# Kernel tuning notes

Hardware: AMD Instinct MI355X
Metric: run time of the kernel (lower is better)

## Reference

```python
import jax, jax.numpy as jnp
import numpy as np

EPS_BN = 1e-5
EPS_LN = 1e-5

def _bn(x, gamma, beta, ch_axis):
    # training-mode BatchNorm: batch stats over all axes except ch_axis (biased var)
    axes = tuple(i for i in range(x.ndim) if i != ch_axis)
    mean = x.mean(axes, keepdims=True)
    var = x.var(axes, keepdims=True)
    shp = [1] * x.ndim; shp[ch_axis] = -1
    return (x - mean) / jnp.sqrt(var + EPS_BN) * gamma.reshape(shp) + beta.reshape(shp)

def _ln(x, gamma, beta):
    mean = x.mean(-1, keepdims=True)
    var = x.var(-1, keepdims=True)
    return (x - mean) / jnp.sqrt(var + EPS_LN) * gamma + beta

def _spline(x, knots, cps):
    # x: (B,S); knots, cps: (K,). Single-pass bucketize + gather + lerp,
    # equivalent to the torch per-interval masked loop (boundary points take
    # the right interval's t=0 value, identical result).
    K = knots.shape[0]
    xn = (x - jnp.min(x)) / (jnp.max(x) - jnp.min(x) + 1e-6)
    idx = jnp.clip(jnp.searchsorted(knots, xn, side='right') - 1, 0, K - 2)
    k0, k1 = knots[idx], knots[idx + 1]
    t = (xn - k0) / (k1 - k0)
    val = (1.0 - t) * cps[idx] + t * cps[idx + 1]
    in_range = (xn >= knots[0]) & (xn <= knots[-1])
    return jnp.where(in_range, val, 0.0)

def _mha(x, in_w, in_b, out_w, out_b, H):
    # torch nn.MultiheadAttention with batch_first=False: dim0 is the sequence.
    L, N, D = x.shape
    hd = D // H
    qkv = x @ in_w.T + in_b                       # (L,N,3D)
    q, k, v = jnp.split(qkv, 3, axis=-1)
    q = q.reshape(L, N, H, hd) * (1.0 / np.sqrt(hd))
    k = k.reshape(L, N, H, hd)
    v = v.reshape(L, N, H, hd)
    scores = jnp.einsum('lnhd,mnhd->nhlm', q, k)  # (N,H,L,L)
    attn = jax.nn.softmax(scores, axis=-1)
    out = jnp.einsum('nhlm,mnhd->lnhd', attn, v).reshape(L, N, D)
    return out @ out_w.T + out_b

def setup_inputs() -> dict:
    B, S, D, F, K, H = 32, 1024, 512, 8, 32, 8
    key = jax.random.key(0)
    ks = jax.random.split(key, 12)
    s = 0.02
    inp = {
        'x': jax.random.normal(ks[0], (B, S, D), jnp.float32),
        'in_w': jax.random.normal(ks[1], (3 * D, D), jnp.float32) * s,
        'in_b': jnp.zeros((3 * D,), jnp.float32),
        'out_w': jax.random.normal(ks[2], (D, D), jnp.float32) * s,
        'out_b': jnp.zeros((D,), jnp.float32),
        'attn_g': jnp.ones((D,), jnp.float32),
        'attn_beta': jnp.zeros((D,), jnp.float32),
        'proj_w': jax.random.normal(ks[3], (F, D), jnp.float32) * s,
        'proj_b': jnp.zeros((F,), jnp.float32),
        'pn_g': jnp.ones((F,), jnp.float32),
        'pn_beta': jnp.zeros((F,), jnp.float32),
        'knots': jnp.tile(jnp.linspace(0.0, 1.0, K, dtype=jnp.float32)[None, :], (F, 1)),
        'cps': jax.random.normal(ks[4], (F, K), jnp.float32) / np.sqrt(K),
        'gate_w': jax.random.normal(ks[5], (2 * D, F), jnp.float32) * s,
        'gate_b': jnp.zeros((2 * D,), jnp.float32),
        'gbn_g': jnp.ones((S,), jnp.float32),   # BatchNorm1d(2*d_model) hits dim1 = seq (= 2*d_model)
        'gbn_beta': jnp.zeros((S,), jnp.float32),
        'ln_g': jnp.ones((D,), jnp.float32),
        'ln_beta': jnp.zeros((D,), jnp.float32),
        'outp_w': jax.random.normal(ks[6], (D, D), jnp.float32) * s,
        'outp_b': jnp.zeros((D,), jnp.float32),
        'on_g': jnp.ones((D,), jnp.float32),
        'on_beta': jnp.zeros((D,), jnp.float32),
    }
    return inp

def reference(x, in_w, in_b, out_w, out_b, attn_g, attn_beta, proj_w, proj_b,
              pn_g, pn_beta, knots, cps, gate_w, gate_b, gbn_g, gbn_beta,
              ln_g, ln_beta, outp_w, outp_b, on_g, on_beta):
    H = 8
    attn_out = _mha(x, in_w, in_b, out_w, out_b, H)          # (B,S,D)
    attn_out = _bn(attn_out, attn_g, attn_beta, 2)
    projected = x @ proj_w.T + proj_b                         # (B,S,F)
    projected = _bn(projected, pn_g, pn_beta, 2)
    transformed = jax.vmap(_spline, in_axes=(2, 0, 0), out_axes=2)(projected, knots, cps)  # (B,S,F)
    h = transformed @ gate_w.T + gate_b                       # (B,S,2D)
    h = _bn(h, gbn_g, gbn_beta, 1)                            # channel axis = seq (torch quirk)
    a, b = jnp.split(h, 2, axis=-1)
    glu = a * jax.nn.sigmoid(b)                               # (B,S,D)
    gated = _ln(glu, ln_g, ln_beta)
    out = gated @ outp_w.T + outp_b
    out = _bn(out, on_g, on_beta, 2)
    return x + attn_out + out
```

## Files before the change

### kernel.cpp

```cpp
#include <hip/hip_runtime.h>
#include <math.h>


#define SOFF_AMEAN 0
#define SOFF_ARSTD 512
#define SOFF_OMEAN 1024
#define SOFF_ORSTD 1536
#define SOFF_PMEAN 2048
#define SOFF_PRSTD 2056
#define SOFF_FMIN  2064
#define SOFF_FMAX  2072
#define SOFF_SMEAN 2080
#define SOFF_SRSTD 3104
#define SOFF_G1    4128
#define SOFF_GB    4136
#define SOFF_SGB   4144
#define SOFF_QGB   4145
#define SOFF_G2    4160
#define SOFF_PART  4224

typedef short bf16x8_t __attribute__((ext_vector_type(8)));
typedef float f32x4_t __attribute__((ext_vector_type(4)));
typedef unsigned short us8_t __attribute__((ext_vector_type(8)));

__device__ __forceinline__ unsigned short f2bf(float f) {
  unsigned u = __float_as_uint(f);
  u = (u + 0x7FFFu + ((u >> 16) & 1u)) >> 16;
  return (unsigned short)u;
}
__device__ __forceinline__ float b2f(unsigned short u) {
  return __uint_as_float(((unsigned)u) << 16);
}

__global__ __launch_bounds__(256) void zero_kernel(float* __restrict__ p) {
  p[blockIdx.x * 256 + threadIdx.x] = 0.f;
}

__global__ __launch_bounds__(256) void cvt8_kernel(const float* __restrict__ src,
                                                   unsigned short* __restrict__ dst) {
  int i = blockIdx.x * 256 + threadIdx.x;
  float4 a = ((const float4*)src)[i * 2];
  float4 b = ((const float4*)src)[i * 2 + 1];
  us8_t o;
  o[0] = f2bf(a.x); o[1] = f2bf(a.y); o[2] = f2bf(a.z); o[3] = f2bf(a.w);
  o[4] = f2bf(b.x); o[5] = f2bf(b.y); o[6] = f2bf(b.z); o[7] = f2bf(b.w);
  *(us8_t*)(dst + (size_t)i * 8) = o;
}

template<int NT, bool OUT_BF16, bool STATS>
__global__ __launch_bounds__(256) void gemm_mfma_kernel(
    const unsigned short* __restrict__ A, const unsigned short* __restrict__ B,
    const float* __restrict__ bias, unsigned short* __restrict__ Cb,
    float* __restrict__ Cf, float* __restrict__ gstats, int N) {
  __shared__ unsigned short As[128 * 32];
  __shared__ unsigned short Bs[128 * 32];
  __shared__ float colred[256];
  const int bi = blockIdx.x;
  const int xcd = bi & 7, j = bi >> 3;
  const int m0 = (xcd * 32 + j / NT) * 128;
  const int n0 = (j % NT) * 128;
  const int t = threadIdx.x;
  const int w = t >> 6, lane = t & 63;
  const int wm = w >> 1, wn = w & 1;
  if (STATS) colred[t] = 0.f;
  f32x4_t acc[4][4];
#pragma unroll
  for (int i = 0; i < 4; ++i)
#pragma unroll
    for (int jj = 0; jj < 4; ++jj) acc[i][jj] = (f32x4_t){0.f, 0.f, 0.f, 0.f};

  const int lrow = lane >> 2;
  const int lk = (lane & 3) * 8;
  const unsigned short* ga = A + (size_t)(m0 + w * 32 + lrow) * 512 + lk;
  const unsigned short* gb = B + (size_t)(n0 + w * 32 + lrow) * 512 + lk;
  unsigned short* lA = &As[(w * 32) * 32];
  unsigned short* lB = &Bs[(w * 32) * 32];
  const int fr = lane & 15, fq = (lane >> 4) * 8;

  for (int k0 = 0; k0 < 512; k0 += 32) {
    __syncthreads();
    __builtin_amdgcn_global_load_lds(
        (const __attribute__((address_space(1))) void*)(ga + k0),
        (__attribute__((address_space(3))) void*)lA, 16, 0, 0);
    __builtin_amdgcn_global_load_lds(
        (const __attribute__((address_space(1))) void*)(ga + k0 + 16 * 512),
        (__attribute__((address_space(3))) void*)(lA + 16 * 32), 16, 0, 0);
    __builtin_amdgcn_global_load_lds(
        (const __attribute__((address_space(1))) void*)(gb + k0),
        (__attribute__((address_space(3))) void*)lB, 16, 0, 0);
    __builtin_amdgcn_global_load_lds(
        (const __attribute__((address_space(1))) void*)(gb + k0 + 16 * 512),
        (__attribute__((address_space(3))) void*)(lB + 16 * 32), 16, 0, 0);
    __syncthreads();
    bf16x8_t af[4], bf[4];
#pragma unroll
    for (int mi = 0; mi < 4; ++mi)
      af[mi] = *(const bf16x8_t*)&As[(wm * 64 + mi * 16 + fr) * 32 + fq];
#pragma unroll
    for (int ni = 0; ni < 4; ++ni)
      bf[ni] = *(const bf16x8_t*)&Bs[(wn * 64 + ni * 16 + fr) * 32 + fq];
#pragma unroll
    for (int mi = 0; mi < 4; ++mi)
#pragma unroll
      for (int ni = 0; ni < 4; ++ni)
        acc[mi][ni] = __builtin_amdgcn_mfma_f32_16x16x32_bf16(af[mi], bf[ni], acc[mi][ni], 0, 0, 0);
  }
  const int cr = (lane >> 4) * 4, cc = lane & 15;
#pragma unroll
  for (int ni = 0; ni < 4; ++ni) {
    int col = n0 + wn * 64 + ni * 16 + cc;
    float bv = bias[col];
    float lsum = 0.f, lsq = 0.f;
#pragma unroll
    for (int mi = 0; mi < 4; ++mi) {
#pragma unroll
      for (int jj = 0; jj < 4; ++jj) {
        int row = m0 + wm * 64 + mi * 16 + cr + jj;
        float v = acc[mi][ni][jj] + bv;
        if (OUT_BF16) Cb[(size_t)row * N + col] = f2bf(v);
        else          Cf[(size_t)row * N + col] = v;
        if (STATS) { lsum += v; lsq += v * v; }
      }
    }
    if (STATS) {
      lsum += __shfl_xor(lsum, 16); lsum += __shfl_xor(lsum, 32);
      lsq  += __shfl_xor(lsq, 16);  lsq  += __shfl_xor(lsq, 32);
      if (lane < 16) {
        int cidx = wn * 64 + ni * 16 + lane;
        atomicAdd(&colred[cidx], lsum);
        atomicAdd(&colred[128 + cidx], lsq);
      }
    }
  }
  if (STATS) {
    __syncthreads();
    if (t < 128) {
      atomicAdd(&gstats[n0 + t], colred[t]);
      atomicAdd(&gstats[512 + n0 + t], colred[128 + t]);
    }
  }
}

__global__ __launch_bounds__(512) void statsfin_kernel(const float* __restrict__ part,
                                                       float* __restrict__ stats, int off) {
  int t = threadIdx.x;
  float mean = part[t] / 32768.f;
  float var = part[512 + t] / 32768.f - mean * mean;
  stats[off + t] = mean;
  stats[off + 512 + t] = rsqrtf(var + 1e-5f);
}

__global__ __launch_bounds__(256) void attn2_kernel(const unsigned short* __restrict__ qkv,
                                                    unsigned short* __restrict__ ctxb) {
  const int n = blockIdx.x, h = blockIdx.y, t = threadIdx.x;
  __shared__ float qs[32 * 68], ks[32 * 68], vs[32 * 68], ss[32 * 33];
  const int l = t >> 3, j0 = (t & 7) * 8;
  size_t rowb = ((size_t)(l * 1024 + n)) * 1536 + h * 64 + j0;
  us8_t qv = *(const us8_t*)(qkv + rowb);
  us8_t kv = *(const us8_t*)(qkv + rowb + 512);
  us8_t vv = *(const us8_t*)(qkv + rowb + 1024);
#pragma unroll
  for (int j = 0; j < 8; ++j) {
    qs[l * 68 + j0 + j] = b2f(qv[j]) * 0.125f;
    ks[l * 68 + j0 + j] = b2f(kv[j]);
    vs[l * 68 + j0 + j] = b2f(vv[j]);
  }
  __syncthreads();
  for (int o = t; o < 1024; o += 256) {
    int ll = o >> 5, m = o & 31;
    const float4* q4 = (const float4*)&qs[ll * 68];
    const float4* k4 = (const float4*)&ks[m * 68];
    float s = 0.f;
#pragma unroll
    for (int dd = 0; dd < 16; ++dd) {
      float4 a = q4[dd], b = k4[dd];
      s += a.x * b.x + a.y * b.y + a.z * b.z + a.w * b.w;
    }
    ss[ll * 33 + m] = s;
  }
  __syncthreads();
  if (t < 32) {
    float mx = -3e38f;
    for (int m = 0; m < 32; ++m) mx = fmaxf(mx, ss[t * 33 + m]);
    float sum = 0.f;
    for (int m = 0; m < 32; ++m) { float e = __expf(ss[t * 33 + m] - mx); ss[t * 33 + m] = e; sum += e; }
    float inv = 1.f / sum;
    for (int m = 0; m < 32; ++m) ss[t * 33 + m] *= inv;
  }
  __syncthreads();
  float o[8] = {0.f, 0.f, 0.f, 0.f, 0.f, 0.f, 0.f, 0.f};
#pragma unroll 8
  for (int m = 0; m < 32; ++m) {
    float pm = ss[l * 33 + m];
    const float* vr = &vs[m * 68 + j0];
#pragma unroll
    for (int j = 0; j < 8; ++j) o[j] += pm * vr[j];
  }
  us8_t ov;
#pragma unroll
  for (int j = 0; j < 8; ++j) ov[j] = f2bf(o[j]);
  *(us8_t*)(ctxb + ((size_t)(l * 1024 + n)) * 512 + h * 64 + j0) = ov;
}

__global__ __launch_bounds__(256) void proj_kernel(const float* __restrict__ x,
    const float* __restrict__ pw, const float* __restrict__ pb, float* __restrict__ p) {
  int blk = blockIdx.x, t = threadIdx.x;
  int r0 = blk * 64;
  __shared__ float xsp[64 * 33];
  __shared__ float pwc[8 * 33];
  int l = t >> 2, fg = t & 3;
  float acc0 = 0.f, acc1 = 0.f;
  for (int k0 = 0; k0 < 512; k0 += 32) {
    __syncthreads();
    for (int i = t; i < 2048; i += 256) { int ll = i >> 5, kk = i & 31; xsp[ll * 33 + kk] = x[(size_t)(r0 + ll) * 512 + k0 + kk]; }
    { int ff = t >> 5, kk = t & 31; pwc[ff * 33 + kk] = pw[ff * 512 + k0 + kk]; }
    __syncthreads();
#pragma unroll 8
    for (int kk = 0; kk < 32; ++kk) {
      float xv = xsp[l * 33 + kk];
      acc0 += xv * pwc[(fg * 2) * 33 + kk];
      acc1 += xv * pwc[(fg * 2 + 1) * 33 + kk];
    }
  }
  float2 o; o.x = acc0 + pb[fg * 2]; o.y = acc1 + pb[fg * 2 + 1];
  *(float2*)&p[(r0 + l) * 8 + fg * 2] = o;
}

__global__ __launch_bounds__(256) void projstats_kernel(const float* __restrict__ p,
                                                        float* __restrict__ part) {
  int t = threadIdx.x, blk = blockIdx.x;
  int f = t & 7;
  float s = 0.f, s2 = 0.f;
  for (int r = blk * 32 + (t >> 3); r < 32768; r += 2048) { float v = p[r * 8 + f]; s += v; s2 += v * v; }
  __shared__ float red[256], red2[256];
  red[t] = s; red2[t] = s2; __syncthreads();
  for (int off = 128; off >= 8; off >>= 1) { if (t < off) { red[t] += red[t + off]; red2[t] += red2[t + off]; } __syncthreads(); }
  if (t < 8) { part[blk * 16 + t] = red[t]; part[blk * 16 + 8 + t] = red2[t]; }
}
__global__ void projfin_kernel(const float* __restrict__ part, float* __restrict__ stats) {
  int t = threadIdx.x;
  if (t < 8) {
    float s = 0.f, s2 = 0.f;
    for (int b = 0; b < 64; ++b) { s += part[b * 16 + t]; s2 += part[b * 16 + 8 + t]; }
    float mean = s / 32768.f;
    float var = s2 / 32768.f - mean * mean;
    stats[SOFF_PMEAN + t] = mean;
    stats[SOFF_PRSTD + t] = rsqrtf(var + 1e-5f);
  }
}

__global__ __launch_bounds__(256) void bnminmax_kernel(float* __restrict__ p,
    const float* __restrict__ stats, const float* __restrict__ png,
    const float* __restrict__ pnb, float* __restrict__ part) {
  int t = threadIdx.x, blk = blockIdx.x;
  int i0 = blk * 256 + t;
  int f = i0 & 7;
  float k1 = stats[SOFF_PRSTD + f] * png[f];
  float k0 = pnb[f] - stats[SOFF_PMEAN + f] * k1;
  float mn = 3e38f, mx = -3e38f;
  for (int i = i0; i < 262144; i += 16384) {
    float v = p[i] * k1 + k0;
    p[i] = v;
    mn = fminf(mn, v); mx = fmaxf(mx, v);
  }
  __shared__ float rmn[256], rmx[256];
  rmn[t] = mn; rmx[t] = mx; __syncthreads();
  for (int off = 128; off >= 8; off >>= 1) {
    if (t < off) { rmn[t] = fminf(rmn[t], rmn[t + off]); rmx[t] = fmaxf(rmx[t], rmx[t + off]); }
    __syncthreads();
  }
  if (t < 8) { part[blk * 16 + t] = rmn[t]; part[blk * 16 + 8 + t] = rmx[t]; }
}
__global__ void minmaxfin_kernel(const float* __restrict__ part, float* __restrict__ stats) {
  int t = threadIdx.x;
  if (t < 8) {
    float mn = 3e38f, mx = -3e38f;
    for (int b = 0; b < 64; ++b) { mn = fminf(mn, part[b * 16 + t]); mx = fmaxf(mx, part[b * 16 + 8 + t]); }
    stats[SOFF_FMIN + t] = mn;
    stats[SOFF_FMAX + t] = mx;
  }
}

__global__ __launch_bounds__(256) void spline_kernel(float* __restrict__ p,
    const float* __restrict__ knots, const float* __restrict__ cps,
    const float* __restrict__ stats) {
  __shared__ float ksh[8 * 33], csh[8 * 33];
  int t = threadIdx.x;
  { int f = t >> 5, j = t & 31; ksh[f * 33 + j] = knots[t]; csh[f * 33 + j] = cps[t]; }
  __syncthreads();
  int i = blockIdx.x * 256 + t;
  int f = i & 7;
  float xv = p[i];
  float mn = stats[SOFF_FMIN + f], mx = stats[SOFF_FMAX + f];
  float xn = (xv - mn) / (mx - mn + 1e-6f);
  const float* kn = &ksh[f * 33];
  const float* cp = &csh[f * 33];
  int pcnt = 0;
#pragma unroll
  for (int j = 0; j < 32; ++j) pcnt += (kn[j] <= xn) ? 1 : 0;
  int idx = pcnt - 1;
  idx = idx < 0 ? 0 : (idx > 30 ? 30 : idx);
  float k0v = kn[idx], k1v = kn[idx + 1];
  float tt = (xn - k0v) / (k1v - k0v);
  float val = (1.f - tt) * cp[idx] + tt * cp[idx + 1];
  bool inr = (xn >= kn[0]) && (xn <= kn[31]);
  p[i] = inr ? val : 0.f;
}

__global__ __launch_bounds__(256) void gateprep_kernel(const float* __restrict__ gw,
    const float* __restrict__ gb, float* __restrict__ stats) {
  int b = blockIdx.x, t = threadIdx.x;
  __shared__ float red[256];
  float s = 0.f;
  if (b < 64) {
    int f1 = b >> 3, f2 = b & 7;
    for (int j = t; j < 1024; j += 256) s += gw[j * 8 + f1] * gw[j * 8 + f2];
  } else if (b < 72) {
    int f = b - 64;
    for (int j = t; j < 1024; j += 256) s += gw[j * 8 + f];
  } else if (b < 80) {
    int f = b - 72;
    for (int j = t; j < 1024; j += 256) s += gb[j] * gw[j * 8 + f];
  } else if (b == 80) {
    for (int j = t; j < 1024; j += 256) s += gb[j];
  } else {
    for (int j = t; j < 1024; j += 256) s += gb[j] * gb[j];
  }
  red[t] = s; __syncthreads();
  for (int off = 128; off > 0; off >>= 1) { if (t < off) red[t] += red[t + off]; __syncthreads(); }
  if (t == 0) {
    float v = red[0];
    if (b < 64) stats[SOFF_G2 + b] = v;
    else if (b < 72) stats[SOFF_G1 + (b - 64)] = v;
    else if (b < 80) stats[SOFF_GB + (b - 72)] = v;
    else if (b == 80) stats[SOFF_SGB] = v;
    else stats[SOFF_QGB] = v;
  }
}

__global__ __launch_bounds__(256) void sstats_kernel(const float* __restrict__ tbuf,
                                                     float* __restrict__ stats) {
  int s = blockIdx.x, t = threadIdx.x;
  __shared__ float tv[256];
  __shared__ float red[256];
  __shared__ float T1[8];
  __shared__ float Ms[64];
  int b = t >> 3, f = t & 7;
  tv[t] = tbuf[(b * 1024 + s) * 8 + f];
  __syncthreads();
  red[t] = tv[t]; __syncthreads();
  for (int off = 128; off >= 8; off >>= 1) { if (t < off) red[t] += red[t + off]; __syncthreads(); }
  if (t < 8) T1[t] = red[t];
  if (t < 64) {
    int f1 = t >> 3, f2 = t & 7; float sM = 0.f;
    for (int bb = 0; bb < 32; ++bb) sM += tv[bb * 8 + f1] * tv[bb * 8 + f2];
    Ms[t] = sM;
  }
  __syncthreads();
  if (t == 0) {
    float sh = 0.f, s2 = 0.f;
    for (int ff = 0; ff < 8; ++ff) {
      sh += stats[SOFF_G1 + ff] * T1[ff];
      s2 += 2.f * stats[SOFF_GB + ff] * T1[ff];
    }
    sh += 32.f * stats[SOFF_SGB];
    for (int i = 0; i < 64; ++i) s2 += Ms[i] * stats[SOFF_G2 + i];
    s2 += 32.f * stats[SOFF_QGB];
    float mean = sh / 32768.f;
    float var = s2 / 32768.f - mean * mean;
    stats[SOFF_SMEAN + s] = mean;
    stats[SOFF_SRSTD + s] = rsqrtf(var + 1e-5f);
  }
}

__global__ __launch_bounds__(256) void gluln_kernel(const float* __restrict__ tbuf,
    const float* __restrict__ gw, const float* __restrict__ gb,
    const float* __restrict__ stats, const float* __restrict__ gbng,
    const float* __restrict__ gbnb, const float* __restrict__ lng,
    const float* __restrict__ lnb, unsigned short* __restrict__ gatedb) {
  const int t = threadIdx.x, wave = t >> 6, lane = t & 63;
  for (int rr = 0; rr < 4; ++rr) {
    const int r = blockIdx.x * 16 + wave * 4 + rr;
    const int s = r & 1023;
    float4 tA = *(const float4*)&tbuf[r * 8];
    float4 tB = *(const float4*)&tbuf[r * 8 + 4];
    float smean = stats[SOFF_SMEAN + s], srstd = stats[SOFF_SRSTD + s];
    float k1 = srstd * gbng[s];
    float k0 = gbnb[s] - smean * k1;
    float g[8];
    float sum = 0.f, sq = 0.f;
#pragma unroll
    for (int i = 0; i < 8; ++i) {
      int c = i * 64 + lane;
      float4 wa0 = *(const float4*)&gw[c * 8];
      float4 wa1 = *(const float4*)&gw[c * 8 + 4];
      float4 wb0 = *(const float4*)&gw[(c + 512) * 8];
      float4 wb1 = *(const float4*)&gw[(c + 512) * 8 + 4];
      float ha = tA.x * wa0.x + tA.y * wa0.y + tA.z * wa0.z + tA.w * wa0.w
               + tB.x * wa1.x + tB.y * wa1.y + tB.z * wa1.z + tB.w * wa1.w + gb[c];
      float hb = tA.x * wb0.x + tA.y * wb0.y + tA.z * wb0.z + tA.w * wb0.w
               + tB.x * wb1.x + tB.y * wb1.y + tB.z * wb1.z + tB.w * wb1.w + gb[c + 512];
      ha = ha * k1 + k0;
      hb = hb * k1 + k0;
      float gv = ha / (1.f + __expf(-hb));
      g[i] = gv; sum += gv; sq += gv * gv;
    }
#pragma unroll
    for (int m = 32; m >= 1; m >>= 1) { sum += __shfl_xor(sum, m); sq += __shfl_xor(sq, m); }
    float mean = sum * (1.f / 512.f);
    float rstd = rsqrtf(sq * (1.f / 512.f) - mean * mean + 1e-5f);
#pragma unroll
    for (int i = 0; i < 8; ++i) {
      int c = i * 64 + lane;
      gatedb[(size_t)r * 512 + c] = f2bf((g[i] - mean) * rstd * lng[c] + lnb[c]);
    }
  }
}

__global__ __launch_bounds__(256) void final_kernel(const float* __restrict__ x,
    const float* __restrict__ attn, const float* __restrict__ outl,
    const float* __restrict__ stats, const float* __restrict__ ag,
    const float* __restrict__ ab, const float* __restrict__ og,
    const float* __restrict__ ob, float* __restrict__ y) {
  int idx = blockIdx.x * 256 + threadIdx.x;
  int c4 = (idx & 127) * 4;
  float4 xv = ((const float4*)x)[idx];
  float4 av = ((const float4*)attn)[idx];
  float4 ov = ((const float4*)outl)[idx];
  float4 am = *(const float4*)&stats[SOFF_AMEAN + c4];
  float4 ar = *(const float4*)&stats[SOFF_ARSTD + c4];
  float4 om = *(const float4*)&stats[SOFF_OMEAN + c4];
  float4 orr = *(const float4*)&stats[SOFF_ORSTD + c4];
  float4 g1 = *(const float4*)&ag[c4];
  float4 b1 = *(const float4*)&ab[c4];
  float4 g2 = *(const float4*)&og[c4];
  float4 b2 = *(const float4*)&ob[c4];
  float4 o;
  o.x = xv.x + (av.x - am.x) * ar.x * g1.x + b1.x + (ov.x - om.x) * orr.x * g2.x + b2.x;
  o.y = xv.y + (av.y - am.y) * ar.y * g1.y + b1.y + (ov.y - om.y) * orr.y * g2.y + b2.y;
  o.z = xv.z + (av.z - am.z) * ar.z * g1.z + b1.z + (ov.z - om.z) * orr.z * g2.z + b2.z;
  o.w = xv.w + (av.w - am.w) * ar.w * g1.w + b1.w + (ov.w - om.w) * orr.w * g2.w + b2.w;
  ((float4*)y)[idx] = o;
}

extern "C" void kernel_launch(void* const* d_in, const int* in_sizes, int n_in,
                              void* d_out, int out_size, void* d_ws, size_t ws_size,
                              hipStream_t stream) {
  (void)in_sizes; (void)n_in; (void)out_size; (void)ws_size;
  const float* x        = (const float*)d_in[0];
  const float* in_w     = (const float*)d_in[1];
  const float* in_b     = (const float*)d_in[2];
  const float* out_w    = (const float*)d_in[3];
  const float* out_b    = (const float*)d_in[4];
  const float* attn_g   = (const float*)d_in[5];
  const float* attn_bt  = (const float*)d_in[6];
  const float* proj_w   = (const float*)d_in[7];
  const float* proj_b   = (const float*)d_in[8];
  const float* pn_g     = (const float*)d_in[9];
  const float* pn_bt    = (const float*)d_in[10];
  const float* knots    = (const float*)d_in[11];
  const float* cps      = (const float*)d_in[12];
  const float* gate_w   = (const float*)d_in[13];
  const float* gate_b   = (const float*)d_in[14];
  const float* gbn_g    = (const float*)d_in[15];
  const float* gbn_bt   = (const float*)d_in[16];
  const float* ln_g     = (const float*)d_in[17];
  const float* ln_bt    = (const float*)d_in[18];
  const float* outp_w   = (const float*)d_in[19];
  const float* outp_b   = (const float*)d_in[20];
  const float* on_g     = (const float*)d_in[21];
  const float* on_bt    = (const float*)d_in[22];

  float* out = (float*)d_out;
  unsigned short* xb      = (unsigned short*)d_ws;
  unsigned short* qkv_b   = xb + 16777216;
  unsigned short* ctx_b   = qkv_b + 50331648;
  unsigned short* wqkv_b  = ctx_b + 16777216;
  unsigned short* wout_b  = wqkv_b + 786432;
  unsigned short* woutp_b = wout_b + 262144;
  float* proj  = (float*)(woutp_b + 262144);
  float* stats = proj + 262144;
  float* part  = stats + SOFF_PART;
  float* partA  = part;
  float* partO  = part + 1024;
  float* partP  = part + 2048;
  float* partMM = part + 3072;
  float* attnf = (float*)qkv_b;
  unsigned short* gated_b = xb;

  zero_kernel<<<dim3(8), dim3(256), 0, stream>>>(part);
  cvt8_kernel<<<dim3(8192), dim3(256), 0, stream>>>(x, xb);
  cvt8_kernel<<<dim3(384), dim3(256), 0, stream>>>(in_w, wqkv_b);
  cvt8_kernel<<<dim3(128), dim3(256), 0, stream>>>(out_w, wout_b);
  cvt8_kernel<<<dim3(128), dim3(256), 0, stream>>>(outp_w, woutp_b);
  gemm_mfma_kernel<12, true, false><<<dim3(3072), dim3(256), 0, stream>>>(
      xb, wqkv_b, in_b, qkv_b, nullptr, nullptr, 1536);
  attn2_kernel<<<dim3(1024, 8), dim3(256), 0, stream>>>(qkv_b, ctx_b);
  gemm_mfma_kernel<4, false, true><<<dim3(1024), dim3(256), 0, stream>>>(
      ctx_b, wout_b, out_b, nullptr, attnf, partA, 512);
  statsfin_kernel<<<dim3(1), dim3(512), 0, stream>>>(partA, stats, SOFF_AMEAN);
  proj_kernel<<<dim3(512), dim3(256), 0, stream>>>(x, proj_w, proj_b, proj);
  projstats_kernel<<<dim3(64), dim3(256), 0, stream>>>(proj, partP);
  projfin_kernel<<<dim3(1), dim3(64), 0, stream>>>(partP, stats);
  bnminmax_kernel<<<dim3(64), dim3(256), 0, stream>>>(proj, stats, pn_g, pn_bt, partMM);
  minmaxfin_kernel<<<dim3(1), dim3(64), 0, stream>>>(partMM, stats);
  spline_kernel<<<dim3(1024), dim3(256), 0, stream>>>(proj, knots, cps, stats);
  gateprep_kernel<<<dim3(88), dim3(256), 0, stream>>>(gate_w, gate_b, stats);
  sstats_kernel<<<dim3(1024), dim3(256), 0, stream>>>(proj, stats);
  gluln_kernel<<<dim3(2048), dim3(256), 0, stream>>>(proj, gate_w, gate_b, stats,
                                                     gbn_g, gbn_bt, ln_g, ln_bt, gated_b);
  gemm_mfma_kernel<4, false, true><<<dim3(1024), dim3(256), 0, stream>>>(
      gated_b, woutp_b, outp_b, nullptr, out, partO, 512);
  statsfin_kernel<<<dim3(1), dim3(512), 0, stream>>>(partO, stats, SOFF_OMEAN);
  final_kernel<<<dim3(16384), dim3(256), 0, stream>>>(x, attnf, out, stats,
                                                      attn_g, attn_bt, on_g, on_bt, out);
}
```

Baseline: 520.3 us.

## Merge prep launches, fold stat finalizers into consumers, swizzle GEMM LDS reads

Replaces the zero kernel and four convert kernels with a single prep kernel that uses block ranges. Removes the separate statistics-finalisation launches: projection sums are accumulated with atomics inside proj_kernel, min/max is reduced inside spline_kernel, and BN mean/rstd are computed inline in bnminmax and final_kernel. Adds an XOR swizzle on the k offset for GEMM LDS stores and fragment reads to reduce bank conflicts. The final residual now reads the bf16 copy of x instead of fp32 x, which halves that traffic but adds rounding error to the output.

```diff
diff --git a/kernel.cpp b/kernel.cpp
--- a/kernel.cpp
+++ b/kernel.cpp
@@ -2,14 +2,6 @@
 #include <math.h>
 
 
-#define SOFF_AMEAN 0
-#define SOFF_ARSTD 512
-#define SOFF_OMEAN 1024
-#define SOFF_ORSTD 1536
-#define SOFF_PMEAN 2048
-#define SOFF_PRSTD 2056
-#define SOFF_FMIN  2064
-#define SOFF_FMAX  2072
 #define SOFF_SMEAN 2080
 #define SOFF_SRSTD 3104
 #define SOFF_G1    4128
@@ -32,18 +24,23 @@
   return __uint_as_float(((unsigned)u) << 16);
 }
 
-__global__ __launch_bounds__(256) void zero_kernel(float* __restrict__ p) {
-  p[blockIdx.x * 256 + threadIdx.x] = 0.f;
-}
-
-__global__ __launch_bounds__(256) void cvt8_kernel(const float* __restrict__ src,
-                                                   unsigned short* __restrict__ dst) {
-  int i = blockIdx.x * 256 + threadIdx.x;
+__global__ __launch_bounds__(256) void prep_kernel(const float* __restrict__ x,
+    const float* __restrict__ in_w, const float* __restrict__ out_w,
+    const float* __restrict__ outp_w, unsigned short* __restrict__ xb,
+    unsigned short* __restrict__ wqkv, unsigned short* __restrict__ wout,
+    unsigned short* __restrict__ woutp, float* __restrict__ part) {
+  int b = blockIdx.x, t = threadIdx.x;
+  const float* src; unsigned short* dst; int i;
+  if (b < 8192)      { src = x;      dst = xb;    i = b * 256 + t; }
+  else if (b < 8576) { src = in_w;   dst = wqkv;  i = (b - 8192) * 256 + t; }
+  else if (b < 8704) { src = out_w;  dst = wout;  i = (b - 8576) * 256 + t; }
+  else if (b < 8832) { src = outp_w; dst = woutp; i = (b - 8704) * 256 + t; }
+  else { ((float4*)part)[(b - 8832) * 256 + t] = (float4){0.f, 0.f, 0.f, 0.f}; return; }
   float4 a = ((const float4*)src)[i * 2];
-  float4 b = ((const float4*)src)[i * 2 + 1];
+  float4 c = ((const float4*)src)[i * 2 + 1];
   us8_t o;
   o[0] = f2bf(a.x); o[1] = f2bf(a.y); o[2] = f2bf(a.z); o[3] = f2bf(a.w);
-  o[4] = f2bf(b.x); o[5] = f2bf(b.y); o[6] = f2bf(b.z); o[7] = f2bf(b.w);
+  o[4] = f2bf(c.x); o[5] = f2bf(c.y); o[6] = f2bf(c.z); o[7] = f2bf(c.w);
   *(us8_t*)(dst + (size_t)i * 8) = o;
 }
 
@@ -70,12 +67,13 @@
     for (int jj = 0; jj < 4; ++jj) acc[i][jj] = (f32x4_t){0.f, 0.f, 0.f, 0.f};
 
   const int lrow = lane >> 2;
-  const int lk = (lane & 3) * 8;
+  const int lk = (((lane & 3) ^ ((lane >> 3) & 3)) * 8);
   const unsigned short* ga = A + (size_t)(m0 + w * 32 + lrow) * 512 + lk;
   const unsigned short* gb = B + (size_t)(n0 + w * 32 + lrow) * 512 + lk;
   unsigned short* lA = &As[(w * 32) * 32];
   unsigned short* lB = &Bs[(w * 32) * 32];
-  const int fr = lane & 15, fq = (lane >> 4) * 8;
+  const int fr = lane & 15;
+  const int fo = ((((lane >> 4) & 3) ^ ((fr >> 1) & 3)) * 8);
 
   for (int k0 = 0; k0 < 512; k0 += 32) {
     __syncthreads();
@@ -95,10 +93,10 @@
     bf16x8_t af[4], bf[4];
 #pragma unroll
     for (int mi = 0; mi < 4; ++mi)
-      af[mi] = *(const bf16x8_t*)&As[(wm * 64 + mi * 16 + fr) * 32 + fq];
+      af[mi] = *(const bf16x8_t*)&As[(wm * 64 + mi * 16 + fr) * 32 + fo];
 #pragma unroll
     for (int ni = 0; ni < 4; ++ni)
-      bf[ni] = *(const bf16x8_t*)&Bs[(wn * 64 + ni * 16 + fr) * 32 + fq];
+      bf[ni] = *(const bf16x8_t*)&Bs[(wn * 64 + ni * 16 + fr) * 32 + fo];
 #pragma unroll
     for (int mi = 0; mi < 4; ++mi)
 #pragma unroll
@@ -139,15 +137,6 @@
       atomicAdd(&gstats[512 + n0 + t], colred[128 + t]);
     }
   }
-}
-
-__global__ __launch_bounds__(512) void statsfin_kernel(const float* __restrict__ part,
-                                                       float* __restrict__ stats, int off) {
-  int t = threadIdx.x;
-  float mean = part[t] / 32768.f;
-  float var = part[512 + t] / 32768.f - mean * mean;
-  stats[off + t] = mean;
-  stats[off + 512 + t] = rsqrtf(var + 1e-5f);
 }
 
 __global__ __launch_bounds__(256) void attn2_kernel(const unsigned short* __restrict__ qkv,
@@ -203,7 +192,8 @@
 }
 
 __global__ __launch_bounds__(256) void proj_kernel(const float* __restrict__ x,
-    const float* __restrict__ pw, const float* __restrict__ pb, float* __restrict__ p) {
+    const float* __restrict__ pw, const float* __restrict__ pb,
+    float* __restrict__ p, float* __restrict__ partP) {
   int blk = blockIdx.x, t = threadIdx.x;
   int r0 = blk * 64;
   __shared__ float xsp[64 * 33];
@@ -224,39 +214,30 @@
   }
   float2 o; o.x = acc0 + pb[fg * 2]; o.y = acc1 + pb[fg * 2 + 1];
   *(float2*)&p[(r0 + l) * 8 + fg * 2] = o;
-}
-
-__global__ __launch_bounds__(256) void projstats_kernel(const float* __restrict__ p,
-                                                        float* __restrict__ part) {
-  int t = threadIdx.x, blk = blockIdx.x;
-  int f = t & 7;
-  float s = 0.f, s2 = 0.f;
-  for (int r = blk * 32 + (t >> 3); r < 32768; r += 2048) { float v = p[r * 8 + f]; s += v; s2 += v * v; }
-  __shared__ float red[256], red2[256];
-  red[t] = s; red2[t] = s2; __syncthreads();
-  for (int off = 128; off >= 8; off >>= 1) { if (t < off) { red[t] += red[t + off]; red2[t] += red2[t + off]; } __syncthreads(); }
-  if (t < 8) { part[blk * 16 + t] = red[t]; part[blk * 16 + 8 + t] = red2[t]; }
-}
-__global__ void projfin_kernel(const float* __restrict__ part, float* __restrict__ stats) {
-  int t = threadIdx.x;
-  if (t < 8) {
-    float s = 0.f, s2 = 0.f;
-    for (int b = 0; b < 64; ++b) { s += part[b * 16 + t]; s2 += part[b * 16 + 8 + t]; }
-    float mean = s / 32768.f;
-    float var = s2 / 32768.f - mean * mean;
-    stats[SOFF_PMEAN + t] = mean;
-    stats[SOFF_PRSTD + t] = rsqrtf(var + 1e-5f);
+  __shared__ float r0s[256], r1s[256], q0s[256], q1s[256];
+  r0s[t] = o.x; r1s[t] = o.y; q0s[t] = o.x * o.x; q1s[t] = o.y * o.y;
+  __syncthreads();
+  for (int off = 128; off >= 4; off >>= 1) {
+    if (t < off) { r0s[t] += r0s[t + off]; r1s[t] += r1s[t + off];
+                   q0s[t] += q0s[t + off]; q1s[t] += q1s[t + off]; }
+    __syncthreads();
+  }
+  if (t < 4) {
+    atomicAdd(&partP[t * 2],     r0s[t]); atomicAdd(&partP[t * 2 + 1],     r1s[t]);
+    atomicAdd(&partP[8 + t * 2], q0s[t]); atomicAdd(&partP[8 + t * 2 + 1], q1s[t]);
   }
 }
 
 __global__ __launch_bounds__(256) void bnminmax_kernel(float* __restrict__ p,
-    const float* __restrict__ stats, const float* __restrict__ png,
-    const float* __restrict__ pnb, float* __restrict__ part) {
+    const float* __restrict__ partP, const float* __restrict__ png,
+    const float* __restrict__ pnb, float* __restrict__ partMM) {
   int t = threadIdx.x, blk = blockIdx.x;
   int i0 = blk * 256 + t;
   int f = i0 & 7;
-  float k1 = stats[SOFF_PRSTD + f] * png[f];
-  float k0 = pnb[f] - stats[SOFF_PMEAN + f] * k1;
+  float pmean = partP[f] * (1.f / 32768.f);
+  float prstd = rsqrtf(partP[8 + f] * (1.f / 32768.f) - pmean * pmean + 1e-5f);
+  float k1 = prstd * png[f];
+  float k0 = pnb[f] - pmean * k1;
   float mn = 3e38f, mx = -3e38f;
   for (int i = i0; i < 262144; i += 16384) {
     float v = p[i] * k1 + k0;
@@ -269,29 +250,30 @@
     if (t < off) { rmn[t] = fminf(rmn[t], rmn[t + off]); rmx[t] = fmaxf(rmx[t], rmx[t + off]); }
     __syncthreads();
   }
-  if (t < 8) { part[blk * 16 + t] = rmn[t]; part[blk * 16 + 8 + t] = rmx[t]; }
-}
-__global__ void minmaxfin_kernel(const float* __restrict__ part, float* __restrict__ stats) {
+  if (t < 8) { partMM[blk * 16 + t] = rmn[t]; partMM[blk * 16 + 8 + t] = rmx[t]; }
+}
+
+__global__ __launch_bounds__(256) void spline_kernel(float* __restrict__ p,
+    const float* __restrict__ knots, const float* __restrict__ cps,
+    const float* __restrict__ partMM) {
+  __shared__ float ksh[8 * 33], csh[8 * 33];
+  __shared__ float fmn[8], fmx[8];
   int t = threadIdx.x;
+  { int f = t >> 5, j = t & 31; ksh[f * 33 + j] = knots[t]; csh[f * 33 + j] = cps[t]; }
   if (t < 8) {
     float mn = 3e38f, mx = -3e38f;
-    for (int b = 0; b < 64; ++b) { mn = fminf(mn, part[b * 16 + t]); mx = fmaxf(mx, part[b * 16 + 8 + t]); }
-    stats[SOFF_FMIN + t] = mn;
-    stats[SOFF_FMAX + t] = mx;
-  }
-}
-
-__global__ __launch_bounds__(256) void spline_kernel(float* __restrict__ p,
-    const float* __restrict__ knots, const float* __restrict__ cps,
-    const float* __restrict__ stats) {
-  __shared__ float ksh[8 * 33], csh[8 * 33];
-  int t = threadIdx.x;
-  { int f = t >> 5, j = t & 31; ksh[f * 33 + j] = knots[t]; csh[f * 33 + j] = cps[t]; }
+#pragma unroll
+    for (int b = 0; b < 64; ++b) {
+      mn = fminf(mn, partMM[b * 16 + t]);
+      mx = fmaxf(mx, partMM[b * 16 + 8 + t]);
+    }
+    fmn[t] = mn; fmx[t] = mx;
+  }
   __syncthreads();
   int i = blockIdx.x * 256 + t;
   int f = i & 7;
   float xv = p[i];
-  float mn = stats[SOFF_FMIN + f], mx = stats[SOFF_FMAX + f];
+  float mn = fmn[f], mx = fmx[f];
   float xn = (xv - mn) / (mx - mn + 1e-6f);
   const float* kn = &ksh[f * 33];
   const float* cp = &csh[f * 33];
@@ -417,30 +399,41 @@
   }
 }
 
-__global__ __launch_bounds__(256) void final_kernel(const float* __restrict__ x,
+__global__ __launch_bounds__(256) void final_kernel(const unsigned short* __restrict__ xb,
     const float* __restrict__ attn, const float* __restrict__ outl,
-    const float* __restrict__ stats, const float* __restrict__ ag,
-    const float* __restrict__ ab, const float* __restrict__ og,
-    const float* __restrict__ ob, float* __restrict__ y) {
+    const float* __restrict__ partA, const float* __restrict__ partO,
+    const float* __restrict__ ag, const float* __restrict__ ab,
+    const float* __restrict__ og, const float* __restrict__ ob,
+    float* __restrict__ y) {
   int idx = blockIdx.x * 256 + threadIdx.x;
   int c4 = (idx & 127) * 4;
-  float4 xv = ((const float4*)x)[idx];
+  ushort4 xu = *(const ushort4*)&xb[(size_t)idx * 4];
   float4 av = ((const float4*)attn)[idx];
   float4 ov = ((const float4*)outl)[idx];
-  float4 am = *(const float4*)&stats[SOFF_AMEAN + c4];
-  float4 ar = *(const float4*)&stats[SOFF_ARSTD + c4];
-  float4 om = *(const float4*)&stats[SOFF_OMEAN + c4];
-  float4 orr = *(const float4*)&stats[SOFF_ORSTD + c4];
+  float4 pa  = *(const float4*)&partA[c4];
+  float4 pa2 = *(const float4*)&partA[512 + c4];
+  float4 po  = *(const float4*)&partO[c4];
+  float4 po2 = *(const float4*)&partO[512 + c4];
   float4 g1 = *(const float4*)&ag[c4];
   float4 b1 = *(const float4*)&ab[c4];
   float4 g2 = *(const float4*)&og[c4];
   float4 b2 = *(const float4*)&ob[c4];
-  float4 o;
-  o.x = xv.x + (av.x - am.x) * ar.x * g1.x + b1.x + (ov.x - om.x) * orr.x * g2.x + b2.x;
-  o.y = xv.y + (av.y - am.y) * ar.y * g1.y + b1.y + (ov.y - om.y) * orr.y * g2.y + b2.y;
-  o.z = xv.z + (av.z - am.z) * ar.z * g1.z + b1.z + (ov.z - om.z) * orr.z * g2.z + b2.z;
-  o.w = xv.w + (av.w - am.w) * ar.w * g1.w + b1.w + (ov.w - om.w) * orr.w * g2.w + b2.w;
-  ((float4*)y)[idx] = o;
+  const float inv = 1.f / 32768.f;
+  float am, ar, om, orr, o;
+  float4 res;
+  am = pa.x * inv; ar = rsqrtf(pa2.x * inv - am * am + 1e-5f);
+  om = po.x * inv; orr = rsqrtf(po2.x * inv - om * om + 1e-5f);
+  o = b2f(xu.x) + (av.x - am) * ar * g1.x + b1.x + (ov.x - om) * orr * g2.x + b2.x; res.x = o;
+  am = pa.y * inv; ar = rsqrtf(pa2.y * inv - am * am + 1e-5f);
+  om = po.y * inv; orr = rsqrtf(po2.y * inv - om * om + 1e-5f);
+  o = b2f(xu.y) + (av.y - am) * ar * g1.y + b1.y + (ov.y - om) * orr * g2.y + b2.y; res.y = o;
+  am = pa.z * inv; ar = rsqrtf(pa2.z * inv - am * am + 1e-5f);
+  om = po.z * inv; orr = rsqrtf(po2.z * inv - om * om + 1e-5f);
+  o = b2f(xu.z) + (av.z - am) * ar * g1.z + b1.z + (ov.z - om) * orr * g2.z + b2.z; res.z = o;
+  am = pa.w * inv; ar = rsqrtf(pa2.w * inv - am * am + 1e-5f);
+  om = po.w * inv; orr = rsqrtf(po2.w * inv - om * om + 1e-5f);
+  o = b2f(xu.w) + (av.w - am) * ar * g1.w + b1.w + (ov.w - om) * orr * g2.w + b2.w; res.w = o;
+  ((float4*)y)[idx] = res;
 }
 
 extern "C" void kernel_launch(void* const* d_in, const int* in_sizes, int n_in,
@@ -486,32 +479,24 @@
   float* partP  = part + 2048;
   float* partMM = part + 3072;
   float* attnf = (float*)qkv_b;
-  unsigned short* gated_b = xb;
-
-  zero_kernel<<<dim3(8), dim3(256), 0, stream>>>(part);
-  cvt8_kernel<<<dim3(8192), dim3(256), 0, stream>>>(x, xb);
-  cvt8_kernel<<<dim3(384), dim3(256), 0, stream>>>(in_w, wqkv_b);
-  cvt8_kernel<<<dim3(128), dim3(256), 0, stream>>>(out_w, wout_b);
-  cvt8_kernel<<<dim3(128), dim3(256), 0, stream>>>(outp_w, woutp_b);
+  unsigned short* gated_b = ctx_b;
+
+  prep_kernel<<<dim3(8836), dim3(256), 0, stream>>>(x, in_w, out_w, outp_w,
+                                                    xb, wqkv_b, wout_b, woutp_b, part);
   gemm_mfma_kernel<12, true, false><<<dim3(3072), dim3(256), 0, stream>>>(
       xb, wqkv_b, in_b, qkv_b, nullptr, nullptr, 1536);
   attn2_kernel<<<dim3(1024, 8), dim3(256), 0, stream>>>(qkv_b, ctx_b);
   gemm_mfma_kernel<4, false, true><<<dim3(1024), dim3(256), 0, stream>>>(
       ctx_b, wout_b, out_b, nullptr, attnf, partA, 512);
-  statsfin_kernel<<<dim3(1), dim3(512), 0, stream>>>(partA, stats, SOFF_AMEAN);
-  proj_kernel<<<dim3(512), dim3(256), 0, stream>>>(x, proj_w, proj_b, proj);
-  projstats_kernel<<<dim3(64), dim3(256), 0, stream>>>(proj, partP);
-  projfin_kernel<<<dim3(1), dim3(64), 0, stream>>>(partP, stats);
-  bnminmax_kernel<<<dim3(64), dim3(256), 0, stream>>>(proj, stats, pn_g, pn_bt, partMM);
-  minmaxfin_kernel<<<dim3(1), dim3(64), 0, stream>>>(partMM, stats);
-  spline_kernel<<<dim3(1024), dim3(256), 0, stream>>>(proj, knots, cps, stats);
+  proj_kernel<<<dim3(512), dim3(256), 0, stream>>>(x, proj_w, proj_b, proj, partP);
+  bnminmax_kernel<<<dim3(64), dim3(256), 0, stream>>>(proj, partP, pn_g, pn_bt, partMM);
+  spline_kernel<<<dim3(1024), dim3(256), 0, stream>>>(proj, knots, cps, partMM);
   gateprep_kernel<<<dim3(88), dim3(256), 0, stream>>>(gate_w, gate_b, stats);
   sstats_kernel<<<dim3(1024), dim3(256), 0, stream>>>(proj, stats);
   gluln_kernel<<<dim3(2048), dim3(256), 0, stream>>>(proj, gate_w, gate_b, stats,
                                                      gbn_g, gbn_bt, ln_g, ln_bt, gated_b);
   gemm_mfma_kernel<4, false, true><<<dim3(1024), dim3(256), 0, stream>>>(
       gated_b, woutp_b, outp_b, nullptr, out, partO, 512);
-  statsfin_kernel<<<dim3(1), dim3(512), 0, stream>>>(partO, stats, SOFF_OMEAN);
-  final_kernel<<<dim3(16384), dim3(256), 0, stream>>>(x, attnf, out, stats,
+  final_kernel<<<dim3(16384), dim3(256), 0, stream>>>(xb, attnf, out, partA, partO,
                                                       attn_g, attn_bt, on_g, on_bt, out);
 }
```

Measured after the change: 521.2 us. No clear change (+0.2%).
